# Kernel tuning notes

Measured on AMD Instinct MI355X. Metric: run time of the kernel, lower is better.

## Reference

```python
import jax, jax.numpy as jnp
import numpy as np

ANCESTOR_INDEX = [[], [0], [0], [0], [0, 1], [0, 2], [0, 3], [0, 1, 4], [0, 2, 5], [0, 3, 6], [0, 1, 4, 7], [0, 2, 5, 8], [0, 3, 6, 9], [0, 3, 6, 9], [0, 3, 6, 9], [0, 3, 6, 9, 12], [0, 3, 6, 9, 13], [0, 3, 6, 9, 14], [0, 3, 6, 9, 13, 16], [0, 3, 6, 9, 14, 17], [0, 3, 6, 9, 13, 16, 18], [0, 3, 6, 9, 14, 17, 19], [0, 3, 6, 9, 13, 16, 18, 20], [0, 3, 6, 9, 14, 17, 19, 21]]
HID = 1024
NP6 = 6
MAXIN = HID + NP6 * 8 + 6


def setup_inputs() -> dict:
    key = jax.random.key(0)
    ks = jax.random.split(key, 18)
    B, T = 2048, 16
    s = 0.02
    inp = {
        'x': jax.random.normal(ks[0], (B, T, 256), jnp.float32),
        'init_pose': jax.random.normal(ks[1], (B, T, 144), jnp.float32) * 0.1,
        'init_shape': jax.random.normal(ks[2], (B, T, 10), jnp.float32) * 0.1,
        'init_cam': jax.random.normal(ks[3], (B, T, 3), jnp.float32) * 0.1,
        'fc1_w': jax.random.normal(ks[4], (HID, 256 + 10), jnp.float32) * s,
        'fc1_b': jnp.zeros((HID,), jnp.float32),
        'fc2_w': jax.random.normal(ks[5], (HID, 256 + 144), jnp.float32) * s,
        'fc2_b': jnp.zeros((HID,), jnp.float32),
        'decshape_w': jax.random.normal(ks[6], (10, HID), jnp.float32) * s,
        'decshape_b': jnp.zeros((10,), jnp.float32),
        'deccam_w': jax.random.normal(ks[7], (3, 2 * HID + 3), jnp.float32) * s,
        'deccam_b': jnp.zeros((3,), jnp.float32),
        'ktd_w': jax.random.normal(ks[8], (24, NP6, MAXIN), jnp.float32) * 0.01,
        'ktd_b': jnp.zeros((24, NP6), jnp.float32),
    }
    return inp


def reference(x, init_pose, init_shape, init_cam, fc1_w, fc1_b, fc2_w, fc2_b,
              decshape_w, decshape_b, deccam_w, deccam_b, ktd_w, ktd_b):
    # fc1 / fc2 (dropout is identity in eval mode)
    xc_shape_cam = jnp.concatenate([x, init_shape], -1) @ fc1_w.T + fc1_b   # [B,T,HID]
    xc_pose_cam = jnp.concatenate([x, init_pose], -1) @ fc2_w.T + fc2_b     # [B,T,HID]

    pose = []
    for j, anc in enumerate(ANCESTOR_INDEX):
        parts = [xc_pose_cam] + [pose[i] for i in anc] + [init_pose[..., j:j + 6]]
        inp = jnp.concatenate(parts, -1)
        pad = MAXIN - inp.shape[-1]
        if pad:
            inp = jnp.pad(inp, ((0, 0), (0, 0), (0, pad)))
        pose.append(jnp.einsum('btd,od->bto', inp, ktd_w[j]) + ktd_b[j])
    pred_pose = jnp.concatenate(pose, -1) + init_pose                        # [B,T,144]

    pred_shape = xc_shape_cam @ decshape_w.T + decshape_b + init_shape      # [B,T,10]
    pred_cam = (jnp.concatenate([xc_pose_cam, xc_shape_cam, init_cam], -1)
                @ deccam_w.T + deccam_b + init_cam)                          # [B,T,3]

    pred_pose = pred_pose.reshape(-1, 144)
    pred_shape = pred_shape.reshape(-1, 10)
    pred_cam = pred_cam.reshape(-1, 3)
    # theta layout matches original output: [cam | pose | shape]
    return jnp.concatenate([pred_cam, pred_pose, pred_shape], -1)           # [B*T,157]
```

## Files before the change

kernel.cpp:

```cpp
#include <hip/hip_runtime.h>
#include <hip/hip_bf16.h>

typedef __attribute__((ext_vector_type(8))) short bf16x8;
typedef __attribute__((ext_vector_type(4))) float f32x4;

static constexpr int ALEN[24] = {0,1,1,1,2,2,2,3,3,3,4,4,4,4,4,5,5,5,6,6,7,7,8,8};
static constexpr int AOFF[24] = {0,0,1,2,3,5,7,9,12,15,18,22,26,30,34,38,43,48,53,59,65,72,79,87};
static constexpr int AFLAT[95] = {
  0, 0, 0,
  0,1, 0,2, 0,3,
  0,1,4, 0,2,5, 0,3,6,
  0,1,4,7, 0,2,5,8, 0,3,6,9, 0,3,6,9, 0,3,6,9,
  0,3,6,9,12, 0,3,6,9,13, 0,3,6,9,14,
  0,3,6,9,13,16, 0,3,6,9,14,17,
  0,3,6,9,13,16,18, 0,3,6,9,14,17,19,
  0,3,6,9,13,16,18,20, 0,3,6,9,14,17,19,21};
static constexpr int LVLN[9] = {1,3,3,3,5,3,2,2,2};
static constexpr int LVLJ[9][5] = {
  {0,0,0,0,0},{1,2,3,0,0},{4,5,6,0,0},{7,8,9,0,0},{10,11,12,13,14},
  {15,16,17,0,0},{18,19,0,0,0},{20,21,0,0,0},{22,23,0,0,0}};

static __device__ __forceinline__ unsigned short f2bf(float f) {
  unsigned int u = __float_as_uint(f);
  u = (u + 0x7fffu + ((u >> 16) & 1u)) >> 16;
  return (unsigned short)u;
}

static __device__ __forceinline__ bf16x8 pack8(float4 lo, float4 hi) {
  bf16x8 r;
  r[0] = (short)f2bf(lo.x); r[1] = (short)f2bf(lo.y);
  r[2] = (short)f2bf(lo.z); r[3] = (short)f2bf(lo.w);
  r[4] = (short)f2bf(hi.x); r[5] = (short)f2bf(hi.y);
  r[6] = (short)f2bf(hi.z); r[7] = (short)f2bf(hi.w);
  return r;
}

__global__ __launch_bounds__(256) void combine_plus(const float* __restrict__ ktd,
                                                    const float* __restrict__ dcw,
                                                    const float* __restrict__ dsw,
                                                    const float* __restrict__ w2,
                                                    const float* __restrict__ b2,
                                                    const float* __restrict__ w1,
                                                    const float* __restrict__ b1,
                                                    float* __restrict__ Gp,
                                                    float* __restrict__ Hp,
                                                    float* __restrict__ S) {
  __shared__ float shpool[5760];
  const int tid = threadIdx.x;

  if (blockIdx.y == 41) {
    if (blockIdx.x >= 4 || blockIdx.z != 0) return;
    float* Sl = shpool;
    const int c0 = blockIdx.x * 36;
    for (int lv = 0; lv < 9; lv++) {
      int units = LVLN[lv] * 54;
      for (int u = tid; u < units; u += 256) {
        int jj = u / 54, rem = u % 54, r = rem / 9, q = rem % 9;
        int j = LVLJ[lv][jj];
        int t = 6 * j + r;
        int cb = c0 + q * 4;
        f32x4 v;
        v[0] = (t == cb)     ? 1.f : 0.f;
        v[1] = (t == cb + 1) ? 1.f : 0.f;
        v[2] = (t == cb + 2) ? 1.f : 0.f;
        v[3] = (t == cb + 3) ? 1.f : 0.f;
        const float* wrow = ktd + (size_t)t * 1078 + 1024;
        for (int a = 0; a < ALEN[j]; a++) {
          int anc = AFLAT[AOFF[j] + a];
          const float* w = wrow + 6 * a;
          #pragma unroll
          for (int k = 0; k < 6; k++) {
            f32x4 s4 = *(const f32x4*)&Sl[(anc * 6 + k) * 40 + q * 4];
            float wk = w[k];
            v[0] += wk * s4[0]; v[1] += wk * s4[1];
            v[2] += wk * s4[2]; v[3] += wk * s4[3];
          }
        }
        *(f32x4*)&Sl[t * 40 + q * 4] = v;
      }
      __syncthreads();
    }
    for (int i = tid; i < 144 * 36; i += 256) {
      int t = i / 36, cc = i % 36;
      S[t * 144 + c0 + cc] = Sl[t * 40 + cc];
    }
    return;
  }

  const bool isH = blockIdx.y >= 37;
  if (isH && blockIdx.x >= 5) return;
  float (*red)[4][64] = (float(*)[4][64])shpool;
  const int w = tid >> 6, lane = tid & 63;
  const int c = blockIdx.x * 64 + lane;
  const int h0 = blockIdx.z * 128 + w * 32;

  const float* vp[4];
  int o0;
  if (!isH) {
    o0 = blockIdx.y * 4;
    #pragma unroll
    for (int oi = 0; oi < 4; oi++) {
      int o = o0 + oi; if (o > 146) o = 146;
      vp[oi] = (o < 144) ? (ktd + (size_t)o * 1078) : (dcw + (size_t)(o - 144) * 2051);
    }
  } else {
    o0 = (blockIdx.y - 37) * 4;
    #pragma unroll
    for (int oi = 0; oi < 4; oi++) {
      int o = o0 + oi; if (o > 12) o = 12;
      vp[oi] = (o < 10) ? (dsw + (size_t)o * 1024) : (dcw + (size_t)(o - 10) * 2051 + 1024);
    }
  }

  float acc[4] = {0.f, 0.f, 0.f, 0.f};
  if (!isH) {
    #pragma unroll 16
    for (int hh = 0; hh < 32; hh++) {
      int h = h0 + hh;
      float wv = (c < 400) ? w2[h * 400 + c] : ((c == 400) ? b2[h] : 0.f);
      #pragma unroll
      for (int oi = 0; oi < 4; oi++) acc[oi] += vp[oi][h] * wv;
    }
  } else {
    #pragma unroll 16
    for (int hh = 0; hh < 32; hh++) {
      int h = h0 + hh;
      float wv = (c < 266) ? w1[h * 266 + c] : ((c == 266) ? b1[h] : 0.f);
      #pragma unroll
      for (int oi = 0; oi < 4; oi++) acc[oi] += vp[oi][h] * wv;
    }
  }

  #pragma unroll
  for (int oi = 0; oi < 4; oi++) red[w][oi][lane] = acc[oi];
  __syncthreads();
  if (w == 0) {
    #pragma unroll
    for (int oi = 0; oi < 4; oi++) {
      int o = o0 + oi;
      float s = red[0][oi][lane] + red[1][oi][lane] + red[2][oi][lane] + red[3][oi][lane];
      if (!isH) {
        if (o < 147 && c <= 400) Gp[(size_t)blockIdx.z * 59200 + o * 401 + c] = s;
      } else {
        if (o < 13 && c <= 266) Hp[(size_t)blockIdx.z * 3520 + o * 267 + c] = s;
      }
    }
  }
}

static __device__ __forceinline__ float gsum(const float* __restrict__ Gp, int t, int c) {
  float s = 0.f;
  #pragma unroll
  for (int z = 0; z < 8; z++) s += Gp[(size_t)z * 59200 + t * 401 + c];
  return s;
}
static __device__ __forceinline__ float hsum(const float* __restrict__ Hp, int t, int c) {
  float s = 0.f;
  #pragma unroll
  for (int z = 0; z < 8; z++) s += Hp[(size_t)z * 3520 + t * 267 + c];
  return s;
}

__global__ __launch_bounds__(256) void assembleM(const float* __restrict__ Gp,
                                                 const float* __restrict__ Hp,
                                                 const float* __restrict__ dcw,
                                                 const float* __restrict__ dcb,
                                                 const float* __restrict__ dsb,
                                                 const float* __restrict__ ktd,
                                                 const float* __restrict__ ktdb,
                                                 float* __restrict__ M0,
                                                 float* __restrict__ C0) {
  int o = blockIdx.x;
  for (int c = threadIdx.x; c < 424; c += 256) {
    float val = 0.f;
    if (c < 413) {
      if (o < 3) {
        if (c < 400) val += gsum(Gp, 144 + o, c);
        if (c < 256) val += hsum(Hp, 10 + o, c);
        if (c >= 400 && c < 410) val += hsum(Hp, 10 + o, 256 + (c - 400));
        if (c >= 410) {
          val += dcw[(size_t)o * 2051 + 2048 + (c - 410)];
          if ((c - 410) == o) val += 1.f;
        }
      } else if (o < 147) {
        int t = o - 3, j = t / 6;
        if (c < 400) val = gsum(Gp, t, c);
        int cj = c - 256 - j;
        if (cj >= 0 && cj < 6) val += ktd[(size_t)t * 1078 + 1024 + 6 * ALEN[j] + cj];
      } else if (o < 157) {
        int s = o - 147;
        if (c < 256) val = hsum(Hp, s, c);
        if (c >= 400 && c < 410) {
          val += hsum(Hp, s, 256 + (c - 400));
          if ((c - 400) == s) val += 1.f;
        }
      }
    }
    M0[o * 424 + c] = val;
  }
  if (threadIdx.x == 0 && o < 157) {
    float bv;
    if (o < 3)        bv = gsum(Gp, 144 + o, 400) + hsum(Hp, 10 + o, 266) + dcb[o];
    else if (o < 147) bv = gsum(Gp, o - 3, 400) + ktdb[o - 3];
    else              bv = hsum(Hp, o - 147, 266) + dsb[o - 147];
    C0[o] = bv;
  }
}

__global__ __launch_bounds__(256) void foldS(const float* __restrict__ S,
                                             const float* __restrict__ M0,
                                             const float* __restrict__ C0,
                                             unsigned short* __restrict__ Mb,
                                             float* __restrict__ Cb) {
  int o = blockIdx.x;
  int c = blockIdx.y * 212 + threadIdx.x;
  bool act = (threadIdx.x < 212) && (c < 424);
  if (o < 3 || o >= 147) {
    if (act) Mb[o * 424 + c] = f2bf(M0[o * 424 + c]);
    if (threadIdx.x == 0 && blockIdx.y == 0) Cb[o] = (o < 157) ? C0[o] : 0.f;
    return;
  }
  int t = o - 3;
  __shared__ float Sl[144];
  if (threadIdx.x < 144) Sl[threadIdx.x] = S[t * 144 + threadIdx.x];
  __syncthreads();
  if (act) {
    float acc = 0.f;
    #pragma unroll 16
    for (int k = 0; k < 144; k++) acc += Sl[k] * M0[(3 + k) * 424 + c];
    if (c == 256 + t) acc += 1.f;
    Mb[o * 424 + c] = f2bf(acc);
  }
  if (threadIdx.x == 0 && blockIdx.y == 0) {
    float acc = 0.f;
    for (int k = 0; k < 144; k++) acc += Sl[k] * C0[3 + k];
    Cb[o] = acc;
  }
}

__global__ __launch_bounds__(512, 2) void main_gemm(const float* __restrict__ x,
                                                    const float* __restrict__ ipose,
                                                    const float* __restrict__ ishape,
                                                    const float* __restrict__ icam,
                                                    const unsigned short* __restrict__ Mb,
                                                    const float* __restrict__ Cb,
                                                    float* __restrict__ out) {
  __shared__ unsigned short Bl[160 * 424];
  const int tid = threadIdx.x;

  {
    const bf16x8* src = (const bf16x8*)Mb;
    bf16x8* dst = (bf16x8*)Bl;
    for (int i = tid; i < 160 * 424 / 8; i += 512) dst[i] = src[i];
  }
  __syncthreads();

  const int w = tid >> 6, lane = tid & 63;
  const int m = lane & 15, g = lane >> 4;
  const int rowbase = blockIdx.x * 128 + w * 16;
  const int row = rowbase + m;
  const float* xr = x + (size_t)row * 256;
  const float* pr = ipose + (size_t)row * 144;

  float4 alo[13], ahi[13];
  #pragma unroll
  for (int k = 0; k < 8; k++) {
    const float* p = xr + k * 32 + g * 8;
    alo[k] = *(const float4*)p; ahi[k] = *(const float4*)(p + 4);
  }
  #pragma unroll
  for (int k = 8; k < 12; k++) {
    const float* p = pr + (k - 8) * 32 + g * 8;
    alo[k] = *(const float4*)p; ahi[k] = *(const float4*)(p + 4);
  }
  if (g < 2) {
    const float* p = pr + 128 + g * 8;
    alo[12] = *(const float4*)p; ahi[12] = *(const float4*)(p + 4);
  } else if (g == 2) {
    const float* p = ishape + (size_t)row * 10;
    alo[12] = make_float4(p[0], p[1], p[2], p[3]);
    ahi[12] = make_float4(p[4], p[5], p[6], p[7]);
  } else {
    const float* p = ishape + (size_t)row * 10;
    const float* q = icam + (size_t)row * 3;
    alo[12] = make_float4(p[8], p[9], q[0], q[1]);
    ahi[12] = make_float4(q[2], 0.f, 0.f, 0.f);
  }
  bf16x8 areg[13];
  #pragma unroll
  for (int k = 0; k < 13; k++) areg[k] = pack8(alo[k], ahi[k]);

  f32x4 acc[10];
  #pragma unroll
  for (int n = 0; n < 10; n++) acc[n] = (f32x4){0.f, 0.f, 0.f, 0.f};

  #pragma unroll
  for (int k = 0; k < 13; k++) {
    #pragma unroll
    for (int n = 0; n < 10; n++) {
      bf16x8 b = *(const bf16x8*)&Bl[(n * 16 + m) * 424 + k * 32 + g * 8];
      acc[n] = __builtin_amdgcn_mfma_f32_16x16x32_bf16(areg[k], b, acc[n], 0, 0, 0);
    }
  }

  #pragma unroll
  for (int n = 0; n < 10; n++) {
    int col = n * 16 + m;
    if (col < 157) {
      float bias = Cb[col];
      #pragma unroll
      for (int q = 0; q < 4; q++)
        out[(size_t)(rowbase + g * 4 + q) * 157 + col] = acc[n][q] + bias;
    }
  }
}

extern "C" void kernel_launch(void* const* d_in, const int* in_sizes, int n_in,
                              void* d_out, int out_size, void* d_ws, size_t ws_size,
                              hipStream_t stream) {
  const float* x      = (const float*)d_in[0];
  const float* ipose  = (const float*)d_in[1];
  const float* ishape = (const float*)d_in[2];
  const float* icam   = (const float*)d_in[3];
  const float* fc1w   = (const float*)d_in[4];
  const float* fc1b   = (const float*)d_in[5];
  const float* fc2w   = (const float*)d_in[6];
  const float* fc2b   = (const float*)d_in[7];
  const float* dsw    = (const float*)d_in[8];
  const float* dsb    = (const float*)d_in[9];
  const float* dcw    = (const float*)d_in[10];
  const float* dcb    = (const float*)d_in[11];
  const float* ktd    = (const float*)d_in[12];
  const float* ktdb   = (const float*)d_in[13];
  int rows = in_sizes[0] / 256;
  float* ws = (float*)d_ws;

  float* Gp = ws;
  float* Hp = ws + 473600;
  float* M0 = ws + 501760;
  float* C0 = ws + 569600;
  float* S  = ws + 569760;
  float* Cb = ws + 590496;
  unsigned short* Mb = (unsigned short*)(ws + 590656);

  combine_plus<<<dim3(7, 42, 8), 256, 0, stream>>>(ktd, dcw, dsw, fc2w, fc2b,
                                                   fc1w, fc1b, Gp, Hp, S);
  assembleM<<<160, 256, 0, stream>>>(Gp, Hp, dcw, dcb, dsb, ktd, ktdb, M0, C0);
  foldS<<<dim3(160, 2), 256, 0, stream>>>(S, M0, C0, Mb, Cb);
  main_gemm<<<rows / 128, 512, 0, stream>>>(x, ipose, ishape, icam, Mb, Cb,
                                            (float*)d_out);
}
```

Before: 57.88 us.

## Split main GEMM output columns across two blocks and overlap B staging with A loads

The main GEMM grid gains a second dimension that splits the 160 output columns into two halves of 80. Each block now stages only half of the folded weight matrix into LDS, which halves shared memory per block and lets the launch bound allow 4 blocks per CU. The global-to-LDS copy of B is issued before the A-row loads, and the barrier moves after them so the two overlap. A loads are packed to bf16 in three groups, with empty asm statements forcing the loads to complete early, which keeps register pressure down. The cost is that every A row is read from global memory and converted twice, once per column half.

```diff
diff --git a/kernel.cpp b/kernel.cpp
--- a/kernel.cpp
+++ b/kernel.cpp
@@ -238,74 +238,111 @@
   }
 }
 
-__global__ __launch_bounds__(512, 2) void main_gemm(const float* __restrict__ x,
+__global__ __launch_bounds__(512, 4) void main_gemm(const float* __restrict__ x,
                                                     const float* __restrict__ ipose,
                                                     const float* __restrict__ ishape,
                                                     const float* __restrict__ icam,
                                                     const unsigned short* __restrict__ Mb,
                                                     const float* __restrict__ Cb,
                                                     float* __restrict__ out) {
-  __shared__ unsigned short Bl[160 * 424];
+  __shared__ alignas(16) unsigned short Bl[80 * 424];
   const int tid = threadIdx.x;
-
-  {
-    const bf16x8* src = (const bf16x8*)Mb;
-    bf16x8* dst = (bf16x8*)Bl;
-    for (int i = tid; i < 160 * 424 / 8; i += 512) dst[i] = src[i];
-  }
-  __syncthreads();
-
   const int w = tid >> 6, lane = tid & 63;
   const int m = lane & 15, g = lane >> 4;
+  const int h = blockIdx.y;
   const int rowbase = blockIdx.x * 128 + w * 16;
   const int row = rowbase + m;
   const float* xr = x + (size_t)row * 256;
   const float* pr = ipose + (size_t)row * 144;
 
-  float4 alo[13], ahi[13];
-  #pragma unroll
-  for (int k = 0; k < 8; k++) {
-    const float* p = xr + k * 32 + g * 8;
-    alo[k] = *(const float4*)p; ahi[k] = *(const float4*)(p + 4);
-  }
-  #pragma unroll
-  for (int k = 8; k < 12; k++) {
-    const float* p = pr + (k - 8) * 32 + g * 8;
-    alo[k] = *(const float4*)p; ahi[k] = *(const float4*)(p + 4);
-  }
-  if (g < 2) {
-    const float* p = pr + 128 + g * 8;
-    alo[12] = *(const float4*)p; ahi[12] = *(const float4*)(p + 4);
-  } else if (g == 2) {
-    const float* p = ishape + (size_t)row * 10;
-    alo[12] = make_float4(p[0], p[1], p[2], p[3]);
-    ahi[12] = make_float4(p[4], p[5], p[6], p[7]);
-  } else {
-    const float* p = ishape + (size_t)row * 10;
-    const float* q = icam + (size_t)row * 3;
-    alo[12] = make_float4(p[8], p[9], q[0], q[1]);
-    ahi[12] = make_float4(q[2], 0.f, 0.f, 0.f);
-  }
+  {
+    const bf16x8* src = (const bf16x8*)(Mb + (size_t)h * 80 * 424);
+    bf16x8* dst = (bf16x8*)Bl;
+    for (int i = tid; i < 80 * 424 / 8; i += 512) dst[i] = src[i];
+  }
+
   bf16x8 areg[13];
-  #pragma unroll
-  for (int k = 0; k < 13; k++) areg[k] = pack8(alo[k], ahi[k]);
-
-  f32x4 acc[10];
-  #pragma unroll
-  for (int n = 0; n < 10; n++) acc[n] = (f32x4){0.f, 0.f, 0.f, 0.f};
+  {
+    float4 lo[5], hi[5];
+    #pragma unroll
+    for (int k = 0; k < 5; k++) {
+      const float* p = xr + k * 32 + g * 8;
+      lo[k] = *(const float4*)p; hi[k] = *(const float4*)(p + 4);
+    }
+    #pragma unroll
+    for (int k = 0; k < 5; k++) {
+      asm volatile("" :: "v"(lo[k].x), "v"(lo[k].y), "v"(lo[k].z), "v"(lo[k].w));
+      asm volatile("" :: "v"(hi[k].x), "v"(hi[k].y), "v"(hi[k].z), "v"(hi[k].w));
+    }
+    #pragma unroll
+    for (int k = 0; k < 5; k++) areg[k] = pack8(lo[k], hi[k]);
+  }
+  {
+    float4 lo[4], hi[4];
+    #pragma unroll
+    for (int k = 0; k < 3; k++) {
+      const float* p = xr + (k + 5) * 32 + g * 8;
+      lo[k] = *(const float4*)p; hi[k] = *(const float4*)(p + 4);
+    }
+    {
+      const float* p = pr + g * 8;
+      lo[3] = *(const float4*)p; hi[3] = *(const float4*)(p + 4);
+    }
+    #pragma unroll
+    for (int k = 0; k < 4; k++) {
+      asm volatile("" :: "v"(lo[k].x), "v"(lo[k].y), "v"(lo[k].z), "v"(lo[k].w));
+      asm volatile("" :: "v"(hi[k].x), "v"(hi[k].y), "v"(hi[k].z), "v"(hi[k].w));
+    }
+    #pragma unroll
+    for (int k = 0; k < 4; k++) areg[k + 5] = pack8(lo[k], hi[k]);
+  }
+  {
+    float4 lo[4], hi[4];
+    #pragma unroll
+    for (int k = 0; k < 3; k++) {
+      const float* p = pr + (k + 1) * 32 + g * 8;
+      lo[k] = *(const float4*)p; hi[k] = *(const float4*)(p + 4);
+    }
+    if (g < 2) {
+      const float* p = pr + 128 + g * 8;
+      lo[3] = *(const float4*)p; hi[3] = *(const float4*)(p + 4);
+    } else if (g == 2) {
+      const float* p = ishape + (size_t)row * 10;
+      lo[3] = make_float4(p[0], p[1], p[2], p[3]);
+      hi[3] = make_float4(p[4], p[5], p[6], p[7]);
+    } else {
+      const float* p = ishape + (size_t)row * 10;
+      const float* q = icam + (size_t)row * 3;
+      lo[3] = make_float4(p[8], p[9], q[0], q[1]);
+      hi[3] = make_float4(q[2], 0.f, 0.f, 0.f);
+    }
+    #pragma unroll
+    for (int k = 0; k < 4; k++) {
+      asm volatile("" :: "v"(lo[k].x), "v"(lo[k].y), "v"(lo[k].z), "v"(lo[k].w));
+      asm volatile("" :: "v"(hi[k].x), "v"(hi[k].y), "v"(hi[k].z), "v"(hi[k].w));
+    }
+    #pragma unroll
+    for (int k = 0; k < 4; k++) areg[k + 9] = pack8(lo[k], hi[k]);
+  }
+
+  __syncthreads();
+
+  f32x4 acc[5];
+  #pragma unroll
+  for (int n = 0; n < 5; n++) acc[n] = (f32x4){0.f, 0.f, 0.f, 0.f};
 
   #pragma unroll
   for (int k = 0; k < 13; k++) {
     #pragma unroll
-    for (int n = 0; n < 10; n++) {
+    for (int n = 0; n < 5; n++) {
       bf16x8 b = *(const bf16x8*)&Bl[(n * 16 + m) * 424 + k * 32 + g * 8];
       acc[n] = __builtin_amdgcn_mfma_f32_16x16x32_bf16(areg[k], b, acc[n], 0, 0, 0);
     }
   }
 
   #pragma unroll
-  for (int n = 0; n < 10; n++) {
-    int col = n * 16 + m;
+  for (int n = 0; n < 5; n++) {
+    int col = h * 80 + n * 16 + m;
     if (col < 157) {
       float bias = Cb[col];
       #pragma unroll
@@ -347,6 +384,6 @@
                                                    fc1w, fc1b, Gp, Hp, S);
   assembleM<<<160, 256, 0, stream>>>(Gp, Hp, dcw, dcb, dsb, ktd, ktdb, M0, C0);
   foldS<<<dim3(160, 2), 256, 0, stream>>>(S, M0, C0, Mb, Cb);
-  main_gemm<<<rows / 128, 512, 0, stream>>>(x, ipose, ishape, icam, Mb, Cb,
-                                            (float*)d_out);
-}
+  main_gemm<<<dim3(rows / 128, 2), 512, 0, stream>>>(x, ipose, ishape, icam,
+                                                     Mb, Cb, (float*)d_out);
+}
```

Measured after the change: 61.85 us. +6.9%, slower.
